# Kernel optimization log

Hardware: AMD Instinct MI355X
Metric: run time of the kernel (lower is better)

Reference implementation:

```python
import jax, jax.numpy as jnp
import numpy as np

WINDOW = 7
PAD = WINDOW // 2
EPS = 1e-8  # torch F.cosine_similarity default eps


def setup_inputs() -> dict:
    key = jax.random.key(0)
    k1, k2, k3 = jax.random.split(key, 3)
    b, c, h, w = 4, 128, 96, 96
    reduced = max(c // 4, 16)  # 32
    x = jax.random.normal(k1, (b, c, h, w), dtype=jnp.float32)
    # 1x1 conv weights (kaiming-uniform-ish scale)
    W_reduce = jax.random.uniform(k2, (reduced, c), dtype=jnp.float32, minval=-1.0, maxval=1.0) * (1.0 / np.sqrt(c))
    W_proj = jax.random.uniform(k3, (c, reduced), dtype=jnp.float32, minval=-1.0, maxval=1.0) * (1.0 / np.sqrt(reduced))
    return {"x": x, "W_reduce": W_reduce, "W_proj": W_proj}


def _local_patches(feat, h, w):
    # feat: (b, r, h, w) -> (b, r, window^2, h, w), unfold ordering (row-major kernel)
    padded = jnp.pad(feat, ((0, 0), (0, 0), (PAD, PAD), (PAD, PAD)))
    return jnp.stack(
        [padded[:, :, i:i + h, j:j + w] for i in range(WINDOW) for j in range(WINDOW)],
        axis=2,
    )


def reference(x, W_reduce, W_proj):
    b, c, h, w = x.shape
    # 1x1 conv reduce
    feat = jnp.einsum('rc,bchw->brhw', W_reduce, x)  # (b, r, h, w)
    patches = _local_patches(feat, h, w)             # (b, r, k2, h, w)
    # cosine similarity along channel dim between center and each patch
    dot = jnp.einsum('brhw,brkhw->bkhw', feat, patches)
    n_center = jnp.sqrt(jnp.sum(feat * feat, axis=1))[:, None]        # (b,1,h,w)
    n_patch = jnp.sqrt(jnp.sum(patches * patches, axis=1))            # (b,k2,h,w)
    sim = dot / jnp.maximum(n_center * n_patch, EPS)                  # (b,k2,h,w)
    att = jax.nn.softmax(sim, axis=1)                                 # over window dim
    corr = jnp.einsum('bkhw,brkhw->brhw', att, patches)               # (b,r,h,w)
    enhanced = jnp.einsum('cr,brhw->bchw', W_proj, corr)              # 1x1 conv proj
    return x + enhanced
```

## Files before the change

kernel.cpp:

```cpp
#include <hip/hip_runtime.h>

#define BB 4
#define CC 128
#define HH 96
#define WWX 96
#define RED 32
#define HW (HH * WWX)
#define NPIX (BB * HW)
#define EPSC 1e-8f

#define TX 32
#define TY 2
#define HX 38
#define HY 8
#define NHALO (HX * HY)
#define PSTRIDE 36

__global__ __launch_bounds__(256) void reduce_kern(
    const float* __restrict__ x, const float* __restrict__ Wr,
    float* __restrict__ feat, float* __restrict__ norms) {
  __shared__ float part[3][64][33];
  int lane = threadIdx.x & 63;
  int cg = __builtin_amdgcn_readfirstlane(threadIdx.x >> 6);
  int pix = blockIdx.x * 64 + lane;
  int b = pix / HW;
  int p = pix - b * HW;
  const float* xp = x + (size_t)b * CC * HW + p;

  float acc[RED];
#pragma unroll
  for (int r = 0; r < RED; ++r) acc[r] = 0.f;

#pragma unroll 8
  for (int i = 0; i < CC / 4; ++i) {
    int c = cg * (CC / 4) + i;
    float xv = xp[(size_t)c * HW];
#pragma unroll
    for (int r = 0; r < RED; ++r) acc[r] = fmaf(Wr[r * CC + c], xv, acc[r]);
  }

  if (cg != 0) {
#pragma unroll
    for (int r = 0; r < RED; ++r) part[cg - 1][lane][r] = acc[r];
  }
  __syncthreads();
  if (cg == 0) {
#pragma unroll
    for (int g = 0; g < 3; ++g)
#pragma unroll
      for (int r = 0; r < RED; ++r) acc[r] += part[g][lane][r];

    float ss = 0.f;
#pragma unroll
    for (int r = 0; r < RED; ++r) ss = fmaf(acc[r], acc[r], ss);
    norms[pix] = sqrtf(ss);

    float4* fo = (float4*)(feat + (size_t)pix * RED);
#pragma unroll
    for (int r4 = 0; r4 < RED / 4; ++r4)
      fo[r4] = make_float4(acc[4 * r4], acc[4 * r4 + 1], acc[4 * r4 + 2], acc[4 * r4 + 3]);
  }
}

__global__ __launch_bounds__(256) void corr_kern(
    const float* __restrict__ x, const float* __restrict__ Wp,
    const float* __restrict__ feat, const float* __restrict__ norms,
    float* __restrict__ out) {
  __shared__ float fbuf[NHALO * PSTRIDE];
  __shared__ float nbuf[NHALO];
  __shared__ float cbuf[64][33];
  int tid = threadIdx.x;
  int b = blockIdx.z;
  int bx = blockIdx.x * TX, by = blockIdx.y * TY;

  for (int s = tid; s < NHALO * 8; s += 256) {
    int px = s >> 3, part = s & 7;
    int hy = px / HX, hx = px - hy * HX;
    int gy = by - 3 + hy, gx = bx - 3 + hx;
    float4 v = make_float4(0.f, 0.f, 0.f, 0.f);
    if ((unsigned)gy < HH && (unsigned)gx < WWX)
      v = *(const float4*)(feat + (size_t)(b * HW + gy * WWX + gx) * RED + part * 4);
    *(float4*)(fbuf + px * PSTRIDE + part * 4) = v;
  }
  for (int n = tid; n < NHALO; n += 256) {
    int hy = n / HX, hx = n - hy * HX;
    int gy = by - 3 + hy, gx = bx - 3 + hx;
    nbuf[n] = ((unsigned)gy < HH && (unsigned)gx < WWX)
                  ? norms[b * HW + gy * WWX + gx] : 0.f;
  }
  __syncthreads();

  int rg = tid & 3;
  int q = tid >> 2;
  int px1 = q & 31, py1 = q >> 5;
  int hidx = (py1 + 3) * HX + (px1 + 3);

  float f[8];
  {
    const float4* fc = (const float4*)(fbuf + hidx * PSTRIDE + rg * 8);
    float4 t0 = fc[0], t1 = fc[1];
    f[0] = t0.x; f[1] = t0.y; f[2] = t0.z; f[3] = t0.w;
    f[4] = t1.x; f[5] = t1.y; f[6] = t1.z; f[7] = t1.w;
  }
  float nc = nbuf[hidx];

  float corr[8];
#pragma unroll
  for (int r = 0; r < 8; ++r) corr[r] = 0.f;
  float l = 0.f;

#pragma unroll
  for (int dy = -3; dy <= 3; ++dy) {
#pragma unroll
    for (int dx = -3; dx <= 3; ++dx) {
      int ho = hidx + dy * HX + dx;
      const float4* fn = (const float4*)(fbuf + ho * PSTRIDE + rg * 8);
      float4 v0 = fn[0], v1 = fn[1];
      float v[8];
      v[0] = v0.x; v[1] = v0.y; v[2] = v0.z; v[3] = v0.w;
      v[4] = v1.x; v[5] = v1.y; v[6] = v1.z; v[7] = v1.w;
      float dot = 0.f;
#pragma unroll
      for (int r = 0; r < 8; ++r) dot = fmaf(f[r], v[r], dot);
      dot += __shfl_xor(dot, 1);
      dot += __shfl_xor(dot, 2);
      float np = nbuf[ho];
      float sim = dot * __builtin_amdgcn_rcpf(fmaxf(nc * np, EPSC));
      float wgt = __expf(sim);
      l += wgt;
#pragma unroll
      for (int r = 0; r < 8; ++r) corr[r] = fmaf(wgt, v[r], corr[r]);
    }
  }

  float invl = __builtin_amdgcn_rcpf(l);
#pragma unroll
  for (int r = 0; r < 8; ++r) cbuf[q][rg * 8 + r] = corr[r] * invl;
  __syncthreads();

  int p2 = tid & 63;
  int cg = __builtin_amdgcn_readfirstlane(tid >> 6);
  int px2 = p2 & 31, py2 = p2 >> 5;
  int pp = (by + py2) * WWX + bx + px2;

  float cr[RED];
#pragma unroll
  for (int r = 0; r < RED; ++r) cr[r] = cbuf[p2][r];

  const float* xc = x + (size_t)b * CC * HW + pp;
  float* oc = out + (size_t)b * CC * HW + pp;
#pragma unroll 4
  for (int i = 0; i < CC / 4; ++i) {
    int c = cg * (CC / 4) + i;
    float a = xc[(size_t)c * HW];
#pragma unroll
    for (int r = 0; r < RED; ++r) a = fmaf(Wp[c * RED + r], cr[r], a);
    oc[(size_t)c * HW] = a;
  }
}

extern "C" void kernel_launch(void* const* d_in, const int* in_sizes, int n_in,
                              void* d_out, int out_size, void* d_ws, size_t ws_size,
                              hipStream_t stream) {
  const float* x  = (const float*)d_in[0];
  const float* Wr = (const float*)d_in[1];
  const float* Wp = (const float*)d_in[2];
  float* out = (float*)d_out;

  float* feat  = (float*)d_ws;
  float* norms = feat + (size_t)NPIX * RED;

  reduce_kern<<<NPIX / 64, 256, 0, stream>>>(x, Wr, feat, norms);

  dim3 g(WWX / TX, HH / TY, BB);
  corr_kern<<<g, 256, 0, stream>>>(x, Wp, feat, norms, out);
}
```

Before: 122.3 us.

## Double threads per block, precompute reciprocal norms, drop LDS padding and reuse buffer

After: 124.1 us. About the same (+1.5%).

```diff
diff --git a/kernel.cpp b/kernel.cpp
--- a/kernel.cpp
+++ b/kernel.cpp
@@ -7,19 +7,16 @@
 #define RED 32
 #define HW (HH * WWX)
 #define NPIX (BB * HW)
-#define EPSC 1e-8f
 
 #define TX 32
 #define TY 2
 #define HX 38
-#define HY 8
-#define NHALO (HX * HY)
-#define PSTRIDE 36
+#define NHALO (HX * 8)
 
-__global__ __launch_bounds__(256) void reduce_kern(
+__global__ __launch_bounds__(512) void reduce_kern(
     const float* __restrict__ x, const float* __restrict__ Wr,
-    float* __restrict__ feat, float* __restrict__ norms) {
-  __shared__ float part[3][64][33];
+    float* __restrict__ feat, float* __restrict__ rnorms) {
+  __shared__ float part[7][64][33];
   int lane = threadIdx.x & 63;
   int cg = __builtin_amdgcn_readfirstlane(threadIdx.x >> 6);
   int pix = blockIdx.x * 64 + lane;
@@ -32,8 +29,8 @@
   for (int r = 0; r < RED; ++r) acc[r] = 0.f;
 
 #pragma unroll 8
-  for (int i = 0; i < CC / 4; ++i) {
-    int c = cg * (CC / 4) + i;
+  for (int i = 0; i < CC / 8; ++i) {
+    int c = cg * (CC / 8) + i;
     float xv = xp[(size_t)c * HW];
 #pragma unroll
     for (int r = 0; r < RED; ++r) acc[r] = fmaf(Wr[r * CC + c], xv, acc[r]);
@@ -46,14 +43,15 @@
   __syncthreads();
   if (cg == 0) {
 #pragma unroll
-    for (int g = 0; g < 3; ++g)
+    for (int g = 0; g < 7; ++g)
 #pragma unroll
       for (int r = 0; r < RED; ++r) acc[r] += part[g][lane][r];
 
     float ss = 0.f;
 #pragma unroll
     for (int r = 0; r < RED; ++r) ss = fmaf(acc[r], acc[r], ss);
-    norms[pix] = sqrtf(ss);
+    float n = sqrtf(ss);
+    rnorms[pix] = (n > 1e-6f) ? __builtin_amdgcn_rcpf(n) : 0.f;
 
     float4* fo = (float4*)(feat + (size_t)pix * RED);
 #pragma unroll
@@ -62,51 +60,44 @@
   }
 }
 
-__global__ __launch_bounds__(256) void corr_kern(
+__global__ __launch_bounds__(512) void corr_kern(
     const float* __restrict__ x, const float* __restrict__ Wp,
-    const float* __restrict__ feat, const float* __restrict__ norms,
+    const float* __restrict__ feat, const float* __restrict__ rnorms,
     float* __restrict__ out) {
-  __shared__ float fbuf[NHALO * PSTRIDE];
+  __shared__ float fbuf[NHALO * RED];
   __shared__ float nbuf[NHALO];
-  __shared__ float cbuf[64][33];
+  float* cbuf = fbuf;
   int tid = threadIdx.x;
   int b = blockIdx.z;
   int bx = blockIdx.x * TX, by = blockIdx.y * TY;
 
-  for (int s = tid; s < NHALO * 8; s += 256) {
+  for (int s = tid; s < NHALO * 8; s += 512) {
     int px = s >> 3, part = s & 7;
     int hy = px / HX, hx = px - hy * HX;
     int gy = by - 3 + hy, gx = bx - 3 + hx;
     float4 v = make_float4(0.f, 0.f, 0.f, 0.f);
     if ((unsigned)gy < HH && (unsigned)gx < WWX)
       v = *(const float4*)(feat + (size_t)(b * HW + gy * WWX + gx) * RED + part * 4);
-    *(float4*)(fbuf + px * PSTRIDE + part * 4) = v;
+    *(float4*)(fbuf + px * RED + part * 4) = v;
   }
-  for (int n = tid; n < NHALO; n += 256) {
+  for (int n = tid; n < NHALO; n += 512) {
     int hy = n / HX, hx = n - hy * HX;
     int gy = by - 3 + hy, gx = bx - 3 + hx;
     nbuf[n] = ((unsigned)gy < HH && (unsigned)gx < WWX)
-                  ? norms[b * HW + gy * WWX + gx] : 0.f;
+                  ? rnorms[b * HW + gy * WWX + gx] : 0.f;
   }
   __syncthreads();
 
-  int rg = tid & 3;
-  int q = tid >> 2;
+  int og = tid & 7;
+  int q = tid >> 3;
   int px1 = q & 31, py1 = q >> 5;
   int hidx = (py1 + 3) * HX + (px1 + 3);
 
-  float f[8];
-  {
-    const float4* fc = (const float4*)(fbuf + hidx * PSTRIDE + rg * 8);
-    float4 t0 = fc[0], t1 = fc[1];
-    f[0] = t0.x; f[1] = t0.y; f[2] = t0.z; f[3] = t0.w;
-    f[4] = t1.x; f[5] = t1.y; f[6] = t1.z; f[7] = t1.w;
-  }
-  float nc = nbuf[hidx];
+  float4 fv = *(const float4*)(fbuf + hidx * RED + og * 4);
+  float rc = nbuf[hidx];
+  float f0 = fv.x * rc, f1 = fv.y * rc, f2 = fv.z * rc, f3 = fv.w * rc;
 
-  float corr[8];
-#pragma unroll
-  for (int r = 0; r < 8; ++r) corr[r] = 0.f;
+  float c0 = 0.f, c1 = 0.f, c2 = 0.f, c3 = 0.f;
   float l = 0.f;
 
 #pragma unroll
@@ -114,28 +105,30 @@
 #pragma unroll
     for (int dx = -3; dx <= 3; ++dx) {
       int ho = hidx + dy * HX + dx;
-      const float4* fn = (const float4*)(fbuf + ho * PSTRIDE + rg * 8);
-      float4 v0 = fn[0], v1 = fn[1];
-      float v[8];
-      v[0] = v0.x; v[1] = v0.y; v[2] = v0.z; v[3] = v0.w;
-      v[4] = v1.x; v[5] = v1.y; v[6] = v1.z; v[7] = v1.w;
-      float dot = 0.f;
-#pragma unroll
-      for (int r = 0; r < 8; ++r) dot = fmaf(f[r], v[r], dot);
+      float4 v = *(const float4*)(fbuf + ho * RED + og * 4);
+      float dot = f0 * v.x;
+      dot = fmaf(f1, v.y, dot);
+      dot = fmaf(f2, v.z, dot);
+      dot = fmaf(f3, v.w, dot);
       dot += __shfl_xor(dot, 1);
       dot += __shfl_xor(dot, 2);
-      float np = nbuf[ho];
-      float sim = dot * __builtin_amdgcn_rcpf(fmaxf(nc * np, EPSC));
+      dot += __shfl_xor(dot, 4);
+      float sim = dot * nbuf[ho];
       float wgt = __expf(sim);
       l += wgt;
-#pragma unroll
-      for (int r = 0; r < 8; ++r) corr[r] = fmaf(wgt, v[r], corr[r]);
+      c0 = fmaf(wgt, v.x, c0);
+      c1 = fmaf(wgt, v.y, c1);
+      c2 = fmaf(wgt, v.z, c2);
+      c3 = fmaf(wgt, v.w, c3);
     }
   }
 
+  __syncthreads();
   float invl = __builtin_amdgcn_rcpf(l);
-#pragma unroll
-  for (int r = 0; r < 8; ++r) cbuf[q][rg * 8 + r] = corr[r] * invl;
+  {
+    float* cb = cbuf + q * 33 + og * 4;
+    cb[0] = c0 * invl; cb[1] = c1 * invl; cb[2] = c2 * invl; cb[3] = c3 * invl;
+  }
   __syncthreads();
 
   int p2 = tid & 63;
@@ -145,13 +138,13 @@
 
   float cr[RED];
 #pragma unroll
-  for (int r = 0; r < RED; ++r) cr[r] = cbuf[p2][r];
+  for (int r = 0; r < RED; ++r) cr[r] = cbuf[p2 * 33 + r];
 
   const float* xc = x + (size_t)b * CC * HW + pp;
   float* oc = out + (size_t)b * CC * HW + pp;
 #pragma unroll 4
-  for (int i = 0; i < CC / 4; ++i) {
-    int c = cg * (CC / 4) + i;
+  for (int i = 0; i < CC / 8; ++i) {
+    int c = cg * (CC / 8) + i;
     float a = xc[(size_t)c * HW];
 #pragma unroll
     for (int r = 0; r < RED; ++r) a = fmaf(Wp[c * RED + r], cr[r], a);
@@ -167,11 +160,11 @@
   const float* Wp = (const float*)d_in[2];
   float* out = (float*)d_out;
 
-  float* feat  = (float*)d_ws;
-  float* norms = feat + (size_t)NPIX * RED;
+  float* feat   = (float*)d_ws;
+  float* rnorms = feat + (size_t)NPIX * RED;
 
-  reduce_kern<<<NPIX / 64, 256, 0, stream>>>(x, Wr, feat, norms);
+  reduce_kern<<<NPIX / 64, 512, 0, stream>>>(x, Wr, feat, rnorms);
 
   dim3 g(WWX / TX, HH / TY, BB);
-  corr_kern<<<g, 256, 0, stream>>>(x, Wp, feat, norms, out);
+  corr_kern<<<g, 512, 0, stream>>>(x, Wp, feat, rnorms, out);
 }
```
